# Optimization experiments

Hardware: AMD Instinct MI355X
Metric: run time of the kernel (lower is better)

Reference implementation:

```python
import jax, jax.numpy as jnp
import numpy as np

B, S, D, DS = 32, 1024, 256, 64
M = 3  # modalities: audio, visual, lexical


def setup_inputs() -> dict:
    key = jax.random.key(0)
    ks = jax.random.split(key, 16)
    w = 0.05
    return {
        "x_audio": jax.random.normal(ks[0], (B, S, D), jnp.float32),
        "x_visual": jax.random.normal(ks[1], (B, S, D), jnp.float32),
        "x_lexical": jax.random.normal(ks[2], (B, S, D), jnp.float32),
        "XW": jax.random.normal(ks[3], (M, DS, D), jnp.float32) * w,
        "Xb": jax.random.normal(ks[4], (M, DS), jnp.float32) * w,
        "HW": jax.random.normal(ks[5], (M, DS, DS), jnp.float32) * w,
        "Hb": jax.random.normal(ks[6], (M, DS), jnp.float32) * w,
        "OW": jax.random.normal(ks[7], (M, D, DS), jnp.float32) * w,
        "Ob": jax.random.normal(ks[8], (M, D), jnp.float32) * w,
        "CW": jax.random.normal(ks[9], (M, M, DS, DS), jnp.float32) * w,
        "W1": jax.random.normal(ks[10], (DS, M * DS), jnp.float32) * w,
        "b1": jax.random.normal(ks[11], (DS,), jnp.float32) * w,
        "W2": jax.random.normal(ks[12], (M * M, DS), jnp.float32) * w,
        "b2": jax.random.normal(ks[13], (M * M,), jnp.float32) * w,
        "ln_g": jnp.ones((M, D), jnp.float32),
        "ln_b": jnp.zeros((M, D), jnp.float32),
    }


def _layernorm(x, g, b, eps=1e-5):
    mu = jnp.mean(x, axis=-1, keepdims=True)
    var = jnp.mean(jnp.square(x - mu), axis=-1, keepdims=True)
    return (x - mu) * jax.lax.rsqrt(var + eps) * g + b


def reference(x_audio, x_visual, x_lexical, XW, Xb, HW, Hb, OW, Ob, CW,
              W1, b1, W2, b2, ln_g, ln_b):
    x = jnp.stack([x_audio, x_visual, x_lexical], axis=0)  # [M,B,S,D]
    xs = x.transpose(2, 0, 1, 3)                            # [S,M,B,D]
    mask = 1.0 - jnp.eye(M, dtype=x.dtype)                  # src != tgt

    def step(h, x_t):
        # h: [M,B,DS], x_t: [M,B,D]
        hc = h.transpose(1, 0, 2).reshape(h.shape[1], M * DS)      # [B, M*DS]
        raw = jnp.tanh(hc @ W1.T + b1) @ W2.T + b2                 # [B, M*M]
        attn = jax.nn.softmax(raw.reshape(-1, M, M), axis=-1)      # [B, tgt, src]
        hproj = jnp.einsum('tsde,sbe->tsbd', CW, h)                # [tgt,src,B,DS]
        coupling = jnp.einsum('bts,ts,tsbd->tbd', attn, mask, hproj)
        su = (jnp.einsum('mde,mbe->mbd', HW, h) + Hb[:, None, :]
              + jnp.einsum('mdk,mbk->mbd', XW, x_t) + Xb[:, None, :]
              + coupling)
        h_new = jax.nn.silu(su)                                    # [M,B,DS]
        y = jnp.einsum('mkd,mbd->mbk', OW, h_new) + Ob[:, None, :]  # [M,B,D]
        return h_new, y

    h0 = jnp.zeros((M, x.shape[1], DS), x.dtype)
    _, ys = jax.lax.scan(step, h0, xs)          # [S,M,B,D]
    out = ys.transpose(1, 2, 0, 3) + x          # residual, [M,B,S,D]
    out = _layernorm(out, ln_g[:, None, None, :], ln_b[:, None, None, :])
    return (out[0], out[1], out[2])
```

## Files before the change

kernel.cpp:

```cpp
#include <hip/hip_runtime.h>
#include <math.h>

#define B_  32
#define S_  1024
#define D_  256
#define DS_ 64
#define M_  3
#define MD_ 192

#define BAR_LGKM() asm volatile("s_waitcnt lgkmcnt(0)\n\ts_barrier" ::: "memory")

__device__ __forceinline__ float rl_f32(float v, int lane) {
    return __uint_as_float(__builtin_amdgcn_readlane(__float_as_uint(v), lane));
}

#define L2E_ 1.4426950408889634f
__device__ __forceinline__ float fast_exp(float x) { return exp2f(x * L2E_); }
__device__ __forceinline__ float fast_tanh(float x) {
    float t = exp2f(x * (2.0f * L2E_));
    return 1.0f - 2.0f * __builtin_amdgcn_rcpf(t + 1.0f);
}

typedef float v4f __attribute__((ext_vector_type(4)));

#define ALD4(dst, p, off) \
    asm volatile("global_load_dwordx4 %0, %1, off offset:" #off \
                 : "=v"(dst) : "v"(p))

#define DECL_W16A(baseptr) \
    v4f W00, W01, W02, W03, W04, W05, W06, W07, \
        W08, W09, W10, W11, W12, W13, W14, W15; \
    { const float* _wp = (baseptr); \
      ALD4(W00, _wp, 0);   ALD4(W01, _wp, 16);  ALD4(W02, _wp, 32);  ALD4(W03, _wp, 48);  \
      ALD4(W04, _wp, 64);  ALD4(W05, _wp, 80);  ALD4(W06, _wp, 96);  ALD4(W07, _wp, 112); \
      ALD4(W08, _wp, 128); ALD4(W09, _wp, 144); ALD4(W10, _wp, 160); ALD4(W11, _wp, 176); \
      ALD4(W12, _wp, 192); ALD4(W13, _wp, 208); ALD4(W14, _wp, 224); ALD4(W15, _wp, 240); \
      asm volatile("s_waitcnt vmcnt(0)" ::: "memory"); }

#define DOT64_PKV(h4, out) { \
    v4f A0 = W00 * (h4)[0]; \
    v4f A1 = W01 * (h4)[1]; \
    v4f A2 = W02 * (h4)[2]; \
    v4f A3 = W03 * (h4)[3]; \
    A0 = __builtin_elementwise_fma(W04, (h4)[4],  A0); \
    A1 = __builtin_elementwise_fma(W05, (h4)[5],  A1); \
    A2 = __builtin_elementwise_fma(W06, (h4)[6],  A2); \
    A3 = __builtin_elementwise_fma(W07, (h4)[7],  A3); \
    A0 = __builtin_elementwise_fma(W08, (h4)[8],  A0); \
    A1 = __builtin_elementwise_fma(W09, (h4)[9],  A1); \
    A2 = __builtin_elementwise_fma(W10, (h4)[10], A2); \
    A3 = __builtin_elementwise_fma(W11, (h4)[11], A3); \
    A0 = __builtin_elementwise_fma(W12, (h4)[12], A0); \
    A1 = __builtin_elementwise_fma(W13, (h4)[13], A1); \
    A2 = __builtin_elementwise_fma(W14, (h4)[14], A2); \
    A3 = __builtin_elementwise_fma(W15, (h4)[15], A3); \
    v4f T = (A0 + A1) + (A2 + A3); \
    out = (T.x + T.y) + (T.z + T.w); \
}

#define DPP_RED3(A, Bv, C) asm volatile( \
    "v_add_f32 %0, %0, %0 row_shr:1 bound_ctrl:0\n\t" \
    "v_add_f32 %1, %1, %1 row_shr:1 bound_ctrl:0\n\t" \
    "v_add_f32 %2, %2, %2 row_shr:1 bound_ctrl:0\n\t" \
    "v_add_f32 %0, %0, %0 row_shr:2 bound_ctrl:0\n\t" \
    "v_add_f32 %1, %1, %1 row_shr:2 bound_ctrl:0\n\t" \
    "v_add_f32 %2, %2, %2 row_shr:2 bound_ctrl:0\n\t" \
    "v_add_f32 %0, %0, %0 row_shr:4 bound_ctrl:0\n\t" \
    "v_add_f32 %1, %1, %1 row_shr:4 bound_ctrl:0\n\t" \
    "v_add_f32 %2, %2, %2 row_shr:4 bound_ctrl:0\n\t" \
    "v_add_f32 %0, %0, %0 row_shr:8 bound_ctrl:0\n\t" \
    "v_add_f32 %1, %1, %1 row_shr:8 bound_ctrl:0\n\t" \
    "v_add_f32 %2, %2, %2 row_shr:8 bound_ctrl:0\n\t" \
    "v_add_f32 %0, %0, %0 row_bcast:15 row_mask:0xa\n\t" \
    "v_add_f32 %1, %1, %1 row_bcast:15 row_mask:0xa\n\t" \
    "v_add_f32 %2, %2, %2 row_bcast:15 row_mask:0xa\n\t" \
    "v_add_f32 %0, %0, %0 row_bcast:31 row_mask:0xc\n\t" \
    "v_add_f32 %1, %1, %1 row_bcast:31 row_mask:0xc\n\t" \
    "v_add_f32 %2, %2, %2 row_bcast:31 row_mask:0xc" \
    : "+v"(A), "+v"(Bv), "+v"(C))

#define DPP_RED4(A, Bv, C, Dv) asm volatile( \
    "v_add_f32 %0, %0, %0 row_shr:1 bound_ctrl:0\n\t" \
    "v_add_f32 %1, %1, %1 row_shr:1 bound_ctrl:0\n\t" \
    "v_add_f32 %2, %2, %2 row_shr:1 bound_ctrl:0\n\t" \
    "v_add_f32 %3, %3, %3 row_shr:1 bound_ctrl:0\n\t" \
    "v_add_f32 %0, %0, %0 row_shr:2 bound_ctrl:0\n\t" \
    "v_add_f32 %1, %1, %1 row_shr:2 bound_ctrl:0\n\t" \
    "v_add_f32 %2, %2, %2 row_shr:2 bound_ctrl:0\n\t" \
    "v_add_f32 %3, %3, %3 row_shr:2 bound_ctrl:0\n\t" \
    "v_add_f32 %0, %0, %0 row_shr:4 bound_ctrl:0\n\t" \
    "v_add_f32 %1, %1, %1 row_shr:4 bound_ctrl:0\n\t" \
    "v_add_f32 %2, %2, %2 row_shr:4 bound_ctrl:0\n\t" \
    "v_add_f32 %3, %3, %3 row_shr:4 bound_ctrl:0\n\t" \
    "v_add_f32 %0, %0, %0 row_shr:8 bound_ctrl:0\n\t" \
    "v_add_f32 %1, %1, %1 row_shr:8 bound_ctrl:0\n\t" \
    "v_add_f32 %2, %2, %2 row_shr:8 bound_ctrl:0\n\t" \
    "v_add_f32 %3, %3, %3 row_shr:8 bound_ctrl:0\n\t" \
    "v_add_f32 %0, %0, %0 row_bcast:15 row_mask:0xa\n\t" \
    "v_add_f32 %1, %1, %1 row_bcast:15 row_mask:0xa\n\t" \
    "v_add_f32 %2, %2, %2 row_bcast:15 row_mask:0xa\n\t" \
    "v_add_f32 %3, %3, %3 row_bcast:15 row_mask:0xa\n\t" \
    "v_add_f32 %0, %0, %0 row_bcast:31 row_mask:0xc\n\t" \
    "v_add_f32 %1, %1, %1 row_bcast:31 row_mask:0xc\n\t" \
    "v_add_f32 %2, %2, %2 row_bcast:31 row_mask:0xc\n\t" \
    "v_add_f32 %3, %3, %3 row_bcast:31 row_mask:0xc" \
    : "+v"(A), "+v"(Bv), "+v"(C), "+v"(Dv))

__global__ __launch_bounds__(256, 2)
void k1_xproj(const float* __restrict__ xa, const float* __restrict__ xv,
              const float* __restrict__ xl, const float* __restrict__ XW,
              const float* __restrict__ Xb, float* __restrict__ xp)
{
    const int m  = blockIdx.z;
    const int b  = blockIdx.y;
    const int t0 = blockIdx.x * 128;
    const float* __restrict__ xm = (m == 0) ? xa : ((m == 1) ? xv : xl);
    const int tid = threadIdx.x;
    const int q = tid >> 6;
    const int d = tid & 63;

    __shared__ __align__(16) float xs[1024];
    __shared__ float part[4][4][64];

    DECL_W16A(XW + ((m * 64 + d) * 256 + q * 64));
    const float xbv = Xb[m * 64 + d];

    for (int g = 0; g < 32; ++g) {
        const int tb = t0 + g * 4;
        reinterpret_cast<v4f*>(xs)[tid] =
            reinterpret_cast<const v4f*>(xm + ((size_t)b * S_ + tb) * D_)[tid];
        __syncthreads();
        #pragma unroll
        for (int tt = 0; tt < 4; ++tt) {
            const v4f* xq = reinterpret_cast<const v4f*>(&xs[tt * 256 + q * 64]);
            float accv;
            DOT64_PKV(xq, accv);
            part[tt][q][d] = accv;
        }
        __syncthreads();
        {
            const int tt = q;
            float ssum = part[tt][0][d] + part[tt][1][d] + part[tt][2][d] + part[tt][3][d] + xbv;
            xp[((size_t)b * S_ + tb + tt) * MD_ + m * 64 + d] = ssum;
        }
    }
}

__global__ __launch_bounds__(768, 1)
void k2_recur(const float* __restrict__ xp, float* __restrict__ hbuf,
              const float* __restrict__ HW, const float* __restrict__ Hb,
              const float* __restrict__ CW, const float* __restrict__ W1,
              const float* __restrict__ b1, const float* __restrict__ W2,
              const float* __restrict__ b2)
{
    const int b    = blockIdx.x;
    const int tid  = threadIdx.x;
    const int w    = tid >> 6;
    const int lane = tid & 63;

    const bool is_gate = (w >= 9);
    const int  m = is_gate ? (w - 9) : (w / 3);
    const int  s = is_gate ? (w - 9) : (w % 3);

    __shared__ __align__(16) float hds[2][MD_];
    __shared__ float parts[12][64];

    if (tid < MD_) hds[0][tid] = 0.f;

    const float* base;
    if (!is_gate) base = (s == m) ? (HW + (m * 64 + lane) * 64)
                                  : (CW + (((m * 3 + s) * 64) + lane) * 64);
    else          base = W1 + lane * MD_ + m * 64;
    DECL_W16A(base);

    float hbv = 0.f, b1v = 0.f;
    float w2r0 = 0.f, w2r1 = 0.f, w2r2 = 0.f, b2v0 = 0.f, b2v1 = 0.f, b2v2 = 0.f;
    float xnext = 0.f;
    if (is_gate) {
        hbv  = Hb[m * 64 + lane];
        b1v  = b1[lane];
        w2r0 = W2[(m * 3 + 0) * 64 + lane];
        w2r1 = W2[(m * 3 + 1) * 64 + lane];
        w2r2 = W2[(m * 3 + 2) * 64 + lane];
        b2v0 = b2[m * 3 + 0]; b2v1 = b2[m * 3 + 1]; b2v2 = b2[m * 3 + 2];
        xnext = xp[((size_t)b * S_) * MD_ + m * 64 + lane];
    }
    const int s1 = (m + 1) % 3, s2 = (m + 2) % 3;
    float hist0 = 0.f, hist1 = 0.f, hist2 = 0.f, hist3 = 0.f;

    __syncthreads();

    for (int t = 0; t < S_; ++t) {
        const int cur = t & 1, nxt = cur ^ 1;

        const float xv = xnext;
        if (is_gate && (t + 1 < S_))
            xnext = xp[((size_t)b * S_ + t + 1) * MD_ + m * 64 + lane];

        const v4f* h4 = reinterpret_cast<const v4f*>(&hds[cur][s * 64]);
        float accv;
        DOT64_PKV(h4, accv);
        parts[w][lane] = accv;
        BAR_LGKM();

        if (is_gate) {
            float pm  = parts[m * 3 + m][lane];
            float pc1 = parts[m * 3 + s1][lane];
            float pc2 = parts[m * 3 + s2][lane];
            float go1 = parts[9 + s1][lane];
            float go2 = parts[9 + s2][lane];

            float z = fast_tanh(b1v + accv + go1 + go2);
            float p0 = w2r0 * z, p1 = w2r1 * z, p2 = w2r2 * z;
            DPP_RED3(p0, p1, p2);
            float r0 = b2v0 + rl_f32(p0, 63);
            float r1 = b2v1 + rl_f32(p1, 63);
            float r2 = b2v2 + rl_f32(p2, 63);
            float mx  = fmaxf(r0, fmaxf(r1, r2));
            float e0  = fast_exp(r0 - mx);
            float e1  = fast_exp(r1 - mx);
            float e2  = fast_exp(r2 - mx);
            float inv = __builtin_amdgcn_rcpf(e0 + e1 + e2);
            float a1v = ((s1 == 1) ? e1 : (s1 == 2) ? e2 : e0) * inv;
            float a2v = ((s2 == 1) ? e1 : (s2 == 2) ? e2 : e0) * inv;

            float suv = xv + hbv + pm + a1v * pc1 + a2v * pc2;
            float hn  = suv * __builtin_amdgcn_rcpf(1.f + fast_exp(-suv));
            hds[nxt][m * 64 + lane] = hn;

            if      ((t & 3) == 0) hist0 = hn;
            else if ((t & 3) == 1) hist1 = hn;
            else if ((t & 3) == 2) hist2 = hn;
            else {
                hist3 = hn;
                float* dst = hbuf + ((size_t)b * S_ + (t - 3)) * MD_ + m * 64 + lane;
                dst[0 * MD_] = hist0; dst[1 * MD_] = hist1;
                dst[2 * MD_] = hist2; dst[3 * MD_] = hist3;
            }
        }
        BAR_LGKM();
    }
}

__global__ __launch_bounds__(256, 2)
void k3_out(const float* __restrict__ xa, const float* __restrict__ xv,
            const float* __restrict__ xl, const float* __restrict__ hbuf,
            const float* __restrict__ OW, const float* __restrict__ Ob,
            const float* __restrict__ lng, const float* __restrict__ lnb,
            float* __restrict__ out)
{
    const int m  = blockIdx.z;
    const int b  = blockIdx.y;
    const int t0 = blockIdx.x * 128;
    const float* __restrict__ xm = (m == 0) ? xa : ((m == 1) ? xv : xl);
    const int k    = threadIdx.x;
    const int wv   = k >> 6;
    const int lane = k & 63;

    __shared__ __align__(16) float hs[4 * 64];
    __shared__ float psum[16], qsum[16];

    DECL_W16A(OW + (m * D_ + k) * DS_);
    const float obv = Ob[m * D_ + k];
    const float gv  = lng[m * D_ + k];
    const float bv  = lnb[m * D_ + k];

    for (int gg = 0; gg < 32; ++gg) {
        const int tb = t0 + gg * 4;
        hs[k] = hbuf[((size_t)b * S_ + tb + (k >> 6)) * MD_ + m * 64 + (k & 63)];
        __syncthreads();

        float v0, v1, v2, v3;
        {
            const v4f* h4 = reinterpret_cast<const v4f*>(&hs[0]);
            float accv; DOT64_PKV(h4, accv);
            v0 = obv + accv + xm[((size_t)b * S_ + tb + 0) * D_ + k];
        }
        {
            const v4f* h4 = reinterpret_cast<const v4f*>(&hs[64]);
            float accv; DOT64_PKV(h4, accv);
            v1 = obv + accv + xm[((size_t)b * S_ + tb + 1) * D_ + k];
        }
        {
            const v4f* h4 = reinterpret_cast<const v4f*>(&hs[128]);
            float accv; DOT64_PKV(h4, accv);
            v2 = obv + accv + xm[((size_t)b * S_ + tb + 2) * D_ + k];
        }
        {
            const v4f* h4 = reinterpret_cast<const v4f*>(&hs[192]);
            float accv; DOT64_PKV(h4, accv);
            v3 = obv + accv + xm[((size_t)b * S_ + tb + 3) * D_ + k];
        }

        float s0 = v0, s1v = v1, s2v = v2, s3 = v3;
        float q0 = v0 * v0, q1 = v1 * v1, q2 = v2 * v2, q3 = v3 * v3;
        DPP_RED4(s0, s1v, s2v, s3);
        DPP_RED4(q0, q1, q2, q3);
        if (lane == 63) {
            psum[wv * 4 + 0] = s0;  psum[wv * 4 + 1] = s1v;
            psum[wv * 4 + 2] = s2v; psum[wv * 4 + 3] = s3;
            qsum[wv * 4 + 0] = q0;  qsum[wv * 4 + 1] = q1;
            qsum[wv * 4 + 2] = q2;  qsum[wv * 4 + 3] = q3;
        }
        __syncthreads();

        const size_t obase = (size_t)m * ((size_t)B_ * S_ * D_) + ((size_t)b * S_ + tb) * D_ + k;
        {
            float ss = psum[0] + psum[4] + psum[8] + psum[12];
            float qq = qsum[0] + qsum[4] + qsum[8] + qsum[12];
            float mu = ss * (1.f / 256.f);
            float var = qq * (1.f / 256.f) - mu * mu;
            float rs = rsqrtf(var + 1e-5f);
            out[obase + 0 * D_] = (v0 - mu) * rs * gv + bv;
        }
        {
            float ss = psum[1] + psum[5] + psum[9] + psum[13];
            float qq = qsum[1] + qsum[5] + qsum[9] + qsum[13];
            float mu = ss * (1.f / 256.f);
            float var = qq * (1.f / 256.f) - mu * mu;
            float rs = rsqrtf(var + 1e-5f);
            out[obase + 1 * D_] = (v1 - mu) * rs * gv + bv;
        }
        {
            float ss = psum[2] + psum[6] + psum[10] + psum[14];
            float qq = qsum[2] + qsum[6] + qsum[10] + qsum[14];
            float mu = ss * (1.f / 256.f);
            float var = qq * (1.f / 256.f) - mu * mu;
            float rs = rsqrtf(var + 1e-5f);
            out[obase + 2 * D_] = (v2 - mu) * rs * gv + bv;
        }
        {
            float ss = psum[3] + psum[7] + psum[11] + psum[15];
            float qq = qsum[3] + qsum[7] + qsum[11] + qsum[15];
            float mu = ss * (1.f / 256.f);
            float var = qq * (1.f / 256.f) - mu * mu;
            float rs = rsqrtf(var + 1e-5f);
            out[obase + 3 * D_] = (v3 - mu) * rs * gv + bv;
        }
    }
}

extern "C" void kernel_launch(void* const* d_in, const int* in_sizes, int n_in,
                              void* d_out, int out_size, void* d_ws, size_t ws_size,
                              hipStream_t stream)
{
    const float* xa  = (const float*)d_in[0];
    const float* xv  = (const float*)d_in[1];
    const float* xl  = (const float*)d_in[2];
    const float* XW  = (const float*)d_in[3];
    const float* Xb  = (const float*)d_in[4];
    const float* HW  = (const float*)d_in[5];
    const float* Hb  = (const float*)d_in[6];
    const float* OW  = (const float*)d_in[7];
    const float* Ob  = (const float*)d_in[8];
    const float* CW  = (const float*)d_in[9];
    const float* W1  = (const float*)d_in[10];
    const float* b1  = (const float*)d_in[11];
    const float* W2  = (const float*)d_in[12];
    const float* b2  = (const float*)d_in[13];
    const float* lng = (const float*)d_in[14];
    const float* lnb = (const float*)d_in[15];
    float* out = (float*)d_out;

    float* xp = (float*)d_ws;
    float* hb = xp + (size_t)B_ * S_ * MD_;

    k1_xproj<<<dim3(8, 32, 3), 256, 0, stream>>>(xa, xv, xl, XW, Xb, xp);
    k2_recur<<<dim3(32), 768, 0, stream>>>(xp, hb, HW, Hb, CW, W1, b1, W2, b2);
    k3_out  <<<dim3(8, 32, 3), 256, 0, stream>>>(xa, xv, xl, hb, OW, Ob, lng, lnb, out);
}
```

Measured before the change: 1.239 ms.

## Halve recurrence block to 6 waves, each computing two 64-wide dot products

The recurrent kernel now uses 384 threads (6 waves) instead of 768 (12 waves). Each wave holds two 64x64 weight sets in registers and computes two dot products that share the same h vector loaded from LDS. The aim is to cut barrier participants and LDS reads of h per step in the latency-bound serial loop. In exchange, register pressure doubles per thread and each wave does twice the FMA work between barriers.

```diff
diff --git a/kernel.cpp b/kernel.cpp
--- a/kernel.cpp
+++ b/kernel.cpp
@@ -27,33 +27,35 @@
     asm volatile("global_load_dwordx4 %0, %1, off offset:" #off \
                  : "=v"(dst) : "v"(p))
 
-#define DECL_W16A(baseptr) \
-    v4f W00, W01, W02, W03, W04, W05, W06, W07, \
-        W08, W09, W10, W11, W12, W13, W14, W15; \
+#define DECL_WSET(P, baseptr) \
+    v4f P##00, P##01, P##02, P##03, P##04, P##05, P##06, P##07, \
+        P##08, P##09, P##10, P##11, P##12, P##13, P##14, P##15; \
     { const float* _wp = (baseptr); \
-      ALD4(W00, _wp, 0);   ALD4(W01, _wp, 16);  ALD4(W02, _wp, 32);  ALD4(W03, _wp, 48);  \
-      ALD4(W04, _wp, 64);  ALD4(W05, _wp, 80);  ALD4(W06, _wp, 96);  ALD4(W07, _wp, 112); \
-      ALD4(W08, _wp, 128); ALD4(W09, _wp, 144); ALD4(W10, _wp, 160); ALD4(W11, _wp, 176); \
-      ALD4(W12, _wp, 192); ALD4(W13, _wp, 208); ALD4(W14, _wp, 224); ALD4(W15, _wp, 240); \
+      ALD4(P##00, _wp, 0);   ALD4(P##01, _wp, 16);  ALD4(P##02, _wp, 32);  ALD4(P##03, _wp, 48);  \
+      ALD4(P##04, _wp, 64);  ALD4(P##05, _wp, 80);  ALD4(P##06, _wp, 96);  ALD4(P##07, _wp, 112); \
+      ALD4(P##08, _wp, 128); ALD4(P##09, _wp, 144); ALD4(P##10, _wp, 160); ALD4(P##11, _wp, 176); \
+      ALD4(P##12, _wp, 192); ALD4(P##13, _wp, 208); ALD4(P##14, _wp, 224); ALD4(P##15, _wp, 240); \
       asm volatile("s_waitcnt vmcnt(0)" ::: "memory"); }
+
+#define EFMA __builtin_elementwise_fma
 
 #define DOT64_PKV(h4, out) { \
     v4f A0 = W00 * (h4)[0]; \
     v4f A1 = W01 * (h4)[1]; \
     v4f A2 = W02 * (h4)[2]; \
     v4f A3 = W03 * (h4)[3]; \
-    A0 = __builtin_elementwise_fma(W04, (h4)[4],  A0); \
-    A1 = __builtin_elementwise_fma(W05, (h4)[5],  A1); \
-    A2 = __builtin_elementwise_fma(W06, (h4)[6],  A2); \
-    A3 = __builtin_elementwise_fma(W07, (h4)[7],  A3); \
-    A0 = __builtin_elementwise_fma(W08, (h4)[8],  A0); \
-    A1 = __builtin_elementwise_fma(W09, (h4)[9],  A1); \
-    A2 = __builtin_elementwise_fma(W10, (h4)[10], A2); \
-    A3 = __builtin_elementwise_fma(W11, (h4)[11], A3); \
-    A0 = __builtin_elementwise_fma(W12, (h4)[12], A0); \
-    A1 = __builtin_elementwise_fma(W13, (h4)[13], A1); \
-    A2 = __builtin_elementwise_fma(W14, (h4)[14], A2); \
-    A3 = __builtin_elementwise_fma(W15, (h4)[15], A3); \
+    A0 = EFMA(W04, (h4)[4],  A0); \
+    A1 = EFMA(W05, (h4)[5],  A1); \
+    A2 = EFMA(W06, (h4)[6],  A2); \
+    A3 = EFMA(W07, (h4)[7],  A3); \
+    A0 = EFMA(W08, (h4)[8],  A0); \
+    A1 = EFMA(W09, (h4)[9],  A1); \
+    A2 = EFMA(W10, (h4)[10], A2); \
+    A3 = EFMA(W11, (h4)[11], A3); \
+    A0 = EFMA(W12, (h4)[12], A0); \
+    A1 = EFMA(W13, (h4)[13], A1); \
+    A2 = EFMA(W14, (h4)[14], A2); \
+    A3 = EFMA(W15, (h4)[15], A3); \
     v4f T = (A0 + A1) + (A2 + A3); \
     out = (T.x + T.y) + (T.z + T.w); \
 }
@@ -122,7 +124,7 @@
     __shared__ __align__(16) float xs[1024];
     __shared__ float part[4][4][64];
 
-    DECL_W16A(XW + ((m * 64 + d) * 256 + q * 64));
+    DECL_WSET(W, XW + ((m * 64 + d) * 256 + q * 64));
     const float xbv = Xb[m * 64 + d];
 
     for (int g = 0; g < 32; ++g) {
@@ -146,7 +148,7 @@
     }
 }
 
-__global__ __launch_bounds__(768, 1)
+__global__ __launch_bounds__(384, 1)
 void k2_recur(const float* __restrict__ xp, float* __restrict__ hbuf,
               const float* __restrict__ HW, const float* __restrict__ Hb,
               const float* __restrict__ CW, const float* __restrict__ W1,
@@ -158,25 +160,37 @@
     const int w    = tid >> 6;
     const int lane = tid & 63;
 
-    const bool is_gate = (w >= 9);
-    const int  m = is_gate ? (w - 9) : (w / 3);
-    const int  s = is_gate ? (w - 9) : (w % 3);
+    const int  seg     = w >> 1;
+    const bool is_tail = (w & 1);
+    const int  m       = seg;
 
     __shared__ __align__(16) float hds[2][MD_];
     __shared__ float parts[12][64];
 
     if (tid < MD_) hds[0][tid] = 0.f;
 
-    const float* base;
-    if (!is_gate) base = (s == m) ? (HW + (m * 64 + lane) * 64)
-                                  : (CW + (((m * 3 + s) * 64) + lane) * 64);
-    else          base = W1 + lane * MD_ + m * 64;
-    DECL_W16A(base);
+    const float* baseA;
+    const float* baseB;
+    int rowA, rowB;
+    if (!is_tail) {
+        baseA = (seg == 0) ? (HW + lane * 64)
+                           : (CW + ((0 * 3 + seg) * 64 + lane) * 64);
+        baseB = (seg == 1) ? (HW + (64 + lane) * 64)
+                           : (CW + ((1 * 3 + seg) * 64 + lane) * 64);
+        rowA = seg; rowB = 3 + seg;
+    } else {
+        baseA = (seg == 2) ? (HW + (128 + lane) * 64)
+                           : (CW + ((2 * 3 + seg) * 64 + lane) * 64);
+        baseB = W1 + lane * MD_ + seg * 64;
+        rowA = 6 + seg; rowB = 9 + seg;
+    }
+    DECL_WSET(W, baseA);
+    DECL_WSET(X, baseB);
 
     float hbv = 0.f, b1v = 0.f;
     float w2r0 = 0.f, w2r1 = 0.f, w2r2 = 0.f, b2v0 = 0.f, b2v1 = 0.f, b2v2 = 0.f;
     float xnext = 0.f;
-    if (is_gate) {
+    if (is_tail) {
         hbv  = Hb[m * 64 + lane];
         b1v  = b1[lane];
         w2r0 = W2[(m * 3 + 0) * 64 + lane];
@@ -194,23 +208,58 @@
         const int cur = t & 1, nxt = cur ^ 1;
 
         const float xv = xnext;
-        if (is_gate && (t + 1 < S_))
+        if (is_tail && (t + 1 < S_))
             xnext = xp[((size_t)b * S_ + t + 1) * MD_ + m * 64 + lane];
 
-        const v4f* h4 = reinterpret_cast<const v4f*>(&hds[cur][s * 64]);
-        float accv;
-        DOT64_PKV(h4, accv);
-        parts[w][lane] = accv;
+        const v4f* h4 = reinterpret_cast<const v4f*>(&hds[cur][seg * 64]);
+        float accA, accB;
+        {
+            v4f A0, A1, A2, A3, B0, B1, B2, B3;
+            {
+                v4f H0 = h4[0], H1 = h4[1], H2 = h4[2], H3 = h4[3];
+                A0 = W00 * H0; B0 = X00 * H0;
+                A1 = W01 * H1; B1 = X01 * H1;
+                A2 = W02 * H2; B2 = X02 * H2;
+                A3 = W03 * H3; B3 = X03 * H3;
+            }
+            {
+                v4f H0 = h4[4], H1 = h4[5], H2 = h4[6], H3 = h4[7];
+                A0 = EFMA(W04, H0, A0); B0 = EFMA(X04, H0, B0);
+                A1 = EFMA(W05, H1, A1); B1 = EFMA(X05, H1, B1);
+                A2 = EFMA(W06, H2, A2); B2 = EFMA(X06, H2, B2);
+                A3 = EFMA(W07, H3, A3); B3 = EFMA(X07, H3, B3);
+            }
+            {
+                v4f H0 = h4[8], H1 = h4[9], H2 = h4[10], H3 = h4[11];
+                A0 = EFMA(W08, H0, A0); B0 = EFMA(X08, H0, B0);
+                A1 = EFMA(W09, H1, A1); B1 = EFMA(X09, H1, B1);
+                A2 = EFMA(W10, H2, A2); B2 = EFMA(X10, H2, B2);
+                A3 = EFMA(W11, H3, A3); B3 = EFMA(X11, H3, B3);
+            }
+            {
+                v4f H0 = h4[12], H1 = h4[13], H2 = h4[14], H3 = h4[15];
+                A0 = EFMA(W12, H0, A0); B0 = EFMA(X12, H0, B0);
+                A1 = EFMA(W13, H1, A1); B1 = EFMA(X13, H1, B1);
+                A2 = EFMA(W14, H2, A2); B2 = EFMA(X14, H2, B2);
+                A3 = EFMA(W15, H3, A3); B3 = EFMA(X15, H3, B3);
+            }
+            v4f TA = (A0 + A1) + (A2 + A3);
+            v4f TB = (B0 + B1) + (B2 + B3);
+            accA = (TA.x + TA.y) + (TA.z + TA.w);
+            accB = (TB.x + TB.y) + (TB.z + TB.w);
+        }
+        parts[rowA][lane] = accA;
+        parts[rowB][lane] = accB;
         BAR_LGKM();
 
-        if (is_gate) {
+        if (is_tail) {
             float pm  = parts[m * 3 + m][lane];
             float pc1 = parts[m * 3 + s1][lane];
             float pc2 = parts[m * 3 + s2][lane];
             float go1 = parts[9 + s1][lane];
             float go2 = parts[9 + s2][lane];
 
-            float z = fast_tanh(b1v + accv + go1 + go2);
+            float z = fast_tanh(b1v + accB + go1 + go2);
             float p0 = w2r0 * z, p1 = w2r1 * z, p2 = w2r2 * z;
             DPP_RED3(p0, p1, p2);
             float r0 = b2v0 + rl_f32(p0, 63);
@@ -260,7 +309,7 @@
     __shared__ __align__(16) float hs[4 * 64];
     __shared__ float psum[16], qsum[16];
 
-    DECL_W16A(OW + (m * D_ + k) * DS_);
+    DECL_WSET(W, OW + (m * D_ + k) * DS_);
     const float obv = Ob[m * D_ + k];
     const float gv  = lng[m * D_ + k];
     const float bv  = lnb[m * D_ + k];
@@ -366,6 +415,6 @@
     float* hb = xp + (size_t)B_ * S_ * MD_;
 
     k1_xproj<<<dim3(8, 32, 3), 256, 0, stream>>>(xa, xv, xl, XW, Xb, xp);
-    k2_recur<<<dim3(32), 768, 0, stream>>>(xp, hb, HW, Hb, CW, W1, b1, W2, b2);
+    k2_recur<<<dim3(32), 384, 0, stream>>>(xp, hb, HW, Hb, CW, W1, b1, W2, b2);
     k3_out  <<<dim3(8, 32, 3), 256, 0, stream>>>(xa, xv, xl, hb, OW, Ob, lng, lnb, out);
 }
```

Result: slower. 1.395 ms (+12.6%).
